# Optimization experiments

Measured on AMD Instinct MI355X. Metric: run time of the kernel, lower is better.

The kernel has to match this reference:

```python
import jax, jax.numpy as jnp
import numpy as np

STEPS = 3
TOP_N = 2
ROUTE_TEMP = 1.5


def setup_inputs() -> dict:
    key = jax.random.key(0)
    ks = jax.random.split(key, 7)
    B, H, W, C = 16, 112, 112, 128
    heads, dh = 2, 64
    hd = heads * dh  # 128
    K = 4
    s_in = 0.02  # keep activations well-scaled through 3 steps
    x = jax.random.normal(ks[0], (B, H, W, C), dtype=jnp.float32)
    Wk = jax.random.normal(ks[1], (C, hd), dtype=jnp.float32) * s_in
    Wv = jax.random.normal(ks[2], (C, hd), dtype=jnp.float32) * s_in
    q = jax.random.normal(ks[3], (heads, dh), dtype=jnp.float32) * 0.1
    Wmlp = jax.random.normal(ks[4], (hd, K), dtype=jnp.float32) * 0.1
    Wb = jax.random.normal(ks[5], (K, C, C), dtype=jnp.float32) * (1.0 / np.sqrt(C))
    alpha = jnp.zeros((), dtype=jnp.float32)  # attn_log_alpha
    return {"x": x, "Wk": Wk, "Wv": Wv, "q": q, "Wmlp": Wmlp, "Wb": Wb, "alpha": alpha}


def _router(x, Wk, Wv, q, Wmlp):
    # AttnPoolRouter: 1x1 conv K/V, single-query-per-head softmax attention pool.
    B, H, W, C = x.shape
    heads, dh = q.shape
    L = H * W
    k = jnp.einsum('bhwc,ce->bhwe', x, Wk).reshape(B, L, heads, dh)  # [B,L,h,d]
    v = jnp.einsum('bhwc,ce->bhwe', x, Wv).reshape(B, L, heads, dh)
    scores = jnp.einsum('hd,blhd->bhl', q, k) / jnp.sqrt(jnp.asarray(dh, x.dtype))
    attn = jax.nn.softmax(scores, axis=-1)                            # [B,h,L]
    pooled = jnp.einsum('bhl,blhd->bhd', attn, v).reshape(B, heads * dh)
    logits = pooled @ Wmlp                                            # [B,K]
    attn_map = attn.mean(axis=1).reshape(B, H, W, 1)                  # [B,H,W,1]
    return logits, attn_map


def reference(x, Wk, Wv, q, Wmlp, Wb, alpha):
    B, H, W, C = x.shape
    K = Wmlp.shape[1]
    scale = jnp.asarray(H * W, x.dtype)
    a = jax.nn.softplus(alpha)
    for _ in range(STEPS):
        logits, attn_map = _router(x, Wk, Wv, q, Wmlp)
        weights = jax.nn.softmax(logits / ROUTE_TEMP, axis=-1)        # [B,K]
        _, top_idx = jax.lax.top_k(weights, TOP_N)                    # [B,top_n]
        top_mask = jax.nn.one_hot(top_idx, K, dtype=weights.dtype).sum(axis=1)
        wm = weights * top_mask
        ws = wm / (wm.sum(axis=-1, keepdims=True) + 1e-9)
        # straight-through: forward = renormalized top-n, gradient flows to full softmax
        wst = ws + jax.lax.stop_gradient(weights - ws)                # [B,K]
        x_mod = x * (1.0 + attn_map * scale * a)                      # [B,H,W,C]
        # all K branch 1x1 convs, combined by straight-through weights
        x = jnp.einsum('bhwc,kcd,bk->bhwd', x_mod, Wb, wst)
    return x
```

## Files before the change

### kernel.cpp

```cpp
#include <hip/hip_runtime.h>
#include <hip/hip_bf16.h>
#include <cstdint>

#define NB 16
#define NC 128
#define NL 12544
#define NHD 128
#define NK 4
#define ROWS (NB*NL)
#define CH 128
#define PCH2 98

typedef unsigned short ushort_t;
typedef __attribute__((ext_vector_type(8))) short bf16x8;
typedef __attribute__((ext_vector_type(4))) float f32x4;

__device__ __forceinline__ float bf2f(unsigned int u){
  union { unsigned int i; float f; } v; v.i = u << 16; return v.f;
}
__device__ __forceinline__ ushort_t f2bf(float f){
  __hip_bfloat16 h = __float2bfloat16(f);
  return *reinterpret_cast<ushort_t*>(&h);
}

__global__ void k_prep(const float* __restrict__ Wk, const float* __restrict__ q,
                       const float* __restrict__ alpha, float* __restrict__ qk,
                       float* __restrict__ scale_a){
  int t = threadIdx.x;
  if (t < NC*2){
    int c = t >> 1, h = t & 1;
    float s = 0.f;
    for (int d = 0; d < 64; ++d) s += Wk[c*NHD + h*64 + d] * q[h*64 + d];
    qk[c*2 + h] = s * 0.125f;
  }
  if (t == 0){
    float a = alpha[0];
    float sp = (a > 20.f) ? a : log1pf(expf(a));
    *scale_a = (float)NL * sp;
  }
}

__global__ void __launch_bounds__(256,4) k_pass1(const float* __restrict__ x,
    const float* __restrict__ qk, float* __restrict__ sraw,
    float* __restrict__ pm, float* __restrict__ pS, float* __restrict__ pP){
  __shared__ __align__(16) ushort_t xs[CH*NC];
  __shared__ float shs0[CH], shs1[CH];
  __shared__ float red[8];
  __shared__ float pmerge[256];
  int wg = ((blockIdx.x & 7) * 196) + (blockIdx.x >> 3);
  int b = wg / PCH2, chunk = wg % PCH2;
  int l0 = chunk*CH;
  int t = threadIdx.x, lane = t & 63, wave = t >> 6;
  int hi = lane >> 4, n16 = lane & 15;

  {
    const float* src = x + ((size_t)b*NL + l0)*NC;
    #pragma unroll
    for (int i = 0; i < 16; ++i){
      int idx = i*1024 + t*4;
      int row = idx >> 7;
      float4 v = *(const float4*)(src + idx);
      unsigned p0 = (unsigned)f2bf(v.x) | ((unsigned)f2bf(v.y) << 16);
      unsigned p1 = (unsigned)f2bf(v.z) | ((unsigned)f2bf(v.w) << 16);
      *(uint2*)((char*)xs + ((idx*2) ^ ((row & 7) << 4))) = make_uint2(p0, p1);
    }
  }
  bf16x8 qfv[4];
  #pragma unroll
  for (int kk = 0; kk < 4; ++kk)
    #pragma unroll
    for (int j = 0; j < 8; ++j){
      int k = kk*32 + hi*8 + j;
      qfv[kk][j] = (n16 < 2) ? (short)f2bf(qk[k*2 + n16]) : (short)0;
    }
  __syncthreads();

  #pragma unroll
  for (int rt2 = 0; rt2 < 2; ++rt2){
    int rt = wave*2 + rt2;
    f32x4 acc = (f32x4){0.f,0.f,0.f,0.f};
    #pragma unroll
    for (int kk = 0; kk < 4; ++kk){
      int row = rt*16 + n16;
      int k = kk*32 + hi*8;
      bf16x8 a = *(const bf16x8*)((const char*)xs + ((row*256 + k*2) ^ ((row & 7) << 4)));
      acc = __builtin_amdgcn_mfma_f32_16x16x32_bf16(a, qfv[kk], acc, 0, 0, 0);
    }
    if (n16 < 2){
      float* dst = n16 ? shs1 : shs0;
      #pragma unroll
      for (int r = 0; r < 4; ++r) dst[rt*16 + hi*4 + r] = acc[r];
    }
  }
  __syncthreads();

  float s0 = -3.4e38f, s1 = -3.4e38f;
  if (t < 128){
    s0 = shs0[t]; s1 = shs1[t];
    sraw[((size_t)b*2+0)*NL + l0 + t] = s0;
    sraw[((size_t)b*2+1)*NL + l0 + t] = s1;
  }
  float m0 = s0, m1 = s1;
  #pragma unroll
  for (int mk = 32; mk; mk >>= 1){ m0 = fmaxf(m0, __shfl_xor(m0, mk)); m1 = fmaxf(m1, __shfl_xor(m1, mk)); }
  if (lane == 0 && wave < 2){ red[wave] = m0; red[2+wave] = m1; }
  __syncthreads();
  float M0 = fmaxf(red[0], red[1]), M1 = fmaxf(red[2], red[3]);
  float e0 = 0.f, e1 = 0.f;
  if (t < 128){ e0 = __expf(s0 - M0); e1 = __expf(s1 - M1); shs0[t] = e0; shs1[t] = e1; }
  float t0 = e0, t1 = e1;
  #pragma unroll
  for (int mk = 32; mk; mk >>= 1){ t0 += __shfl_xor(t0, mk); t1 += __shfl_xor(t1, mk); }
  if (lane == 0 && wave < 2){ red[4+wave] = t0; red[6+wave] = t1; }
  __syncthreads();
  if (t == 0){
    pm[(b*2+0)*PCH2 + chunk] = M0; pm[(b*2+1)*PCH2 + chunk] = M1;
    pS[(b*2+0)*PCH2 + chunk] = red[4]+red[5];
    pS[(b*2+1)*PCH2 + chunk] = red[6]+red[7];
  }

  int h = t >> 7, half = (t >> 6) & 1, cp = t & 63;
  const float* es = h ? shs1 : shs0;
  float a0 = 0.f, a1 = 0.f;
  #pragma unroll 4
  for (int i = 0; i < 64; ++i){
    int l = half*64 + i;
    float e = es[l];
    unsigned u = *(const unsigned*)((const char*)xs + ((l*256 + 4*cp) ^ ((l & 7) << 4)));
    a0 += e * bf2f(u & 0xffffu);
    a1 += e * bf2f(u >> 16);
  }
  __syncthreads();
  if (half){ pmerge[h*128 + cp*2] = a0; pmerge[h*128 + cp*2 + 1] = a1; }
  __syncthreads();
  if (!half){
    a0 += pmerge[h*128 + cp*2];
    a1 += pmerge[h*128 + cp*2 + 1];
    float2 w; w.x = a0; w.y = a1;
    *(float2*)&pP[(((size_t)b*PCH2 + chunk)*2 + h)*NC + 2*cp] = w;
  }
}

__global__ void k_combine(const float* __restrict__ pm, const float* __restrict__ pS,
    const float* __restrict__ pP, const float* __restrict__ Wv,
    const float* __restrict__ Wmlp, const float* __restrict__ Wb,
    ushort_t* __restrict__ WT, float* __restrict__ amS){
  int b = blockIdx.x, t = threadIdx.x, lane = t & 63, wave = t >> 6;
  __shared__ float w98[2][PCH2];
  __shared__ float pxs[2][NC];
  __shared__ float vpool[NHD];
  __shared__ float wts[NK];
  __shared__ float mSh[4];
  __shared__ float wcomb[NC*129];

  if (wave < 2){
    int h = wave;
    const float* pmh = pm + (b*2+h)*PCH2;
    const float* pSh = pS + (b*2+h)*PCH2;
    float m = -3.4e38f;
    for (int j = lane; j < PCH2; j += 64) m = fmaxf(m, pmh[j]);
    #pragma unroll
    for (int mk = 32; mk; mk >>= 1) m = fmaxf(m, __shfl_xor(m, mk));
    float S = 0.f;
    for (int j = lane; j < PCH2; j += 64) S += pSh[j] * __expf(pmh[j] - m);
    #pragma unroll
    for (int mk = 32; mk; mk >>= 1) S += __shfl_xor(S, mk);
    for (int j = lane; j < PCH2; j += 64) w98[h][j] = __expf(pmh[j] - m);
    if (lane == 0){
      float iS = 1.f/S;
      mSh[h] = m; mSh[2+h] = iS;
      amS[(b*2+h)*2 + 0] = m; amS[(b*2+h)*2 + 1] = iS;
    }
  }
  __syncthreads();
  {
    int h = t >> 7, c = t & 127;
    float s = 0.f;
    #pragma unroll 2
    for (int j = 0; j < PCH2; ++j) s += pP[(((size_t)b*PCH2 + j)*2 + h)*NC + c] * w98[h][j];
    pxs[h][c] = s * mSh[2+h];
  }
  __syncthreads();
  if (t < NHD){
    int h = t >> 6, d = t & 63;
    float s = 0.f;
    for (int c = 0; c < NC; ++c) s += pxs[h][c] * Wv[c*NHD + h*64 + d];
    vpool[t] = s;
  }
  __syncthreads();
  if (t < NK){
    float s = 0.f;
    for (int e = 0; e < NHD; ++e) s += vpool[e] * Wmlp[e*NK + t];
    wts[t] = s * (1.0f/1.5f);
  }
  __syncthreads();
  if (t == 0){
    float m = fmaxf(fmaxf(wts[0], wts[1]), fmaxf(wts[2], wts[3]));
    float e0 = __expf(wts[0]-m), e1 = __expf(wts[1]-m), e2 = __expf(wts[2]-m), e3 = __expf(wts[3]-m);
    float inv = 1.f/(e0+e1+e2+e3);
    wts[0] = e0*inv; wts[1] = e1*inv; wts[2] = e2*inv; wts[3] = e3*inv;
  }
  __syncthreads();
  float w0 = wts[0], w1 = wts[1], w2 = wts[2], w3 = wts[3];
  for (int idx = t; idx < NC*NC; idx += 256){
    int c = idx >> 7, d = idx & 127;
    const float* wb = Wb + (size_t)c*NC + d;
    wcomb[c*129 + d] = w0*wb[0] + w1*wb[NC*NC] + w2*wb[2*NC*NC] + w3*wb[3*NC*NC];
  }
  __syncthreads();
  for (int idx = t; idx < NC*NHD; idx += 256){
    int d = idx >> 7, c = idx & 127;
    WT[(size_t)b*NC*NHD + d*NC + c] = f2bf(wcomb[c*129 + d]);
  }
}

template<typename XIN, typename XOUT, bool STATS>
__global__ void __launch_bounds__(256,2) k_gemm(const XIN* __restrict__ xin,
    const ushort_t* __restrict__ WT, const float* __restrict__ qkg,
    float* __restrict__ sraw, const float* __restrict__ amS,
    const float* __restrict__ scale_a, XOUT* __restrict__ xout,
    float* __restrict__ pm, float* __restrict__ pS, float* __restrict__ pP){
  __shared__ __align__(16) ushort_t lA[CH*NC];
  __shared__ __align__(16) ushort_t lB[NC*NHD];
  __shared__ float sqk[256];
  __shared__ float shs0[CH], shs1[CH];
  __shared__ float red[8];
  __shared__ float pacc[4][2][NC];
  int wg = ((blockIdx.x & 7) * 196) + (blockIdx.x >> 3);
  int b = wg / PCH2, chunk = wg % PCH2;
  int l0 = chunk*CH;
  int t = threadIdx.x;
  float sa = scale_a[0]*0.5f;
  float am0 = amS[(b*2+0)*2+0], ai0 = amS[(b*2+0)*2+1];
  float am1 = amS[(b*2+1)*2+0], ai1 = amS[(b*2+1)*2+1];
  const float* s0p = sraw + ((size_t)b*2 + 0)*NL + l0;
  const float* s1p = sraw + ((size_t)b*2 + 1)*NL + l0;

  if (STATS){ sqk[t] = qkg[t]; }

  {
    const ushort_t* src = WT + (size_t)b*NC*NHD;
    #pragma unroll
    for (int i = 0; i < 8; ++i){
      int idx = i*2048 + t*8;
      int d = idx >> 7;
      uint4 v = *(const uint4*)(src + idx);
      *(uint4*)((char*)lB + ((idx*2) ^ ((d & 7) << 4))) = v;
    }
  }
  if constexpr (sizeof(XIN) == 4){
    const float* src = (const float*)xin + ((size_t)b*NL + l0)*NC;
    #pragma unroll
    for (int i = 0; i < 16; ++i){
      int idx = i*1024 + t*4;
      int row = idx >> 7;
      float4 v = *(const float4*)(src + idx);
      float mod = 1.f + sa*(__expf(s0p[row]-am0)*ai0 + __expf(s1p[row]-am1)*ai1);
      unsigned p0 = (unsigned)f2bf(v.x*mod) | ((unsigned)f2bf(v.y*mod) << 16);
      unsigned p1 = (unsigned)f2bf(v.z*mod) | ((unsigned)f2bf(v.w*mod) << 16);
      *(uint2*)((char*)lA + ((idx*2) ^ ((row & 7) << 4))) = make_uint2(p0, p1);
    }
  } else {
    const ushort_t* src = (const ushort_t*)xin + ((size_t)b*NL + l0)*NC;
    #pragma unroll
    for (int i = 0; i < 8; ++i){
      int idx = i*2048 + t*8;
      int row = idx >> 7;
      uint4 v = *(const uint4*)(src + idx);
      float mod = 1.f + sa*(__expf(s0p[row]-am0)*ai0 + __expf(s1p[row]-am1)*ai1);
      unsigned vv[4] = {v.x, v.y, v.z, v.w};
      unsigned r[4];
      #pragma unroll
      for (int j = 0; j < 4; ++j){
        float lo = bf2f(vv[j] & 0xffffu)*mod, hi2 = bf2f(vv[j] >> 16)*mod;
        r[j] = (unsigned)f2bf(lo) | ((unsigned)f2bf(hi2) << 16);
      }
      *(uint4*)((char*)lA + ((idx*2) ^ ((row & 7) << 4))) = make_uint4(r[0], r[1], r[2], r[3]);
    }
  }
  __syncthreads();

  int lane = t & 63, wave = t >> 6;
  int trow = lane & 15, kg = lane >> 4;
  int r0 = wave*32;
  f32x4 acc[2][8];
  #pragma unroll
  for (int m = 0; m < 2; ++m)
    #pragma unroll
    for (int n = 0; n < 8; ++n) acc[m][n] = (f32x4){0.f,0.f,0.f,0.f};

  #pragma unroll
  for (int kk = 0; kk < 4; ++kk){
    int k = kk*32 + kg*8;
    int ra0 = r0 + trow, ra1 = r0 + 16 + trow;
    bf16x8 a0 = *(const bf16x8*)((const char*)lA + ((ra0*256 + k*2) ^ ((ra0 & 7) << 4)));
    bf16x8 a1 = *(const bf16x8*)((const char*)lA + ((ra1*256 + k*2) ^ ((ra1 & 7) << 4)));
    #pragma unroll
    for (int nt = 0; nt < 8; ++nt){
      int col = nt*16 + trow;
      bf16x8 bf = *(const bf16x8*)((const char*)lB + ((col*256 + k*2) ^ ((col & 7) << 4)));
      acc[0][nt] = __builtin_amdgcn_mfma_f32_16x16x32_bf16(a0, bf, acc[0][nt], 0, 0, 0);
      acc[1][nt] = __builtin_amdgcn_mfma_f32_16x16x32_bf16(a1, bf, acc[1][nt], 0, 0, 0);
    }
  }

  size_t base = ((size_t)b*NL + l0)*NC;
  #pragma unroll
  for (int m = 0; m < 2; ++m)
    #pragma unroll
    for (int nt = 0; nt < 8; ++nt)
      #pragma unroll
      for (int r = 0; r < 4; ++r){
        int row = r0 + m*16 + kg*4 + r;
        int col = nt*16 + trow;
        float v = acc[m][nt][r];
        if constexpr (sizeof(XOUT) == 4) ((float*)xout)[base + (size_t)row*NC + col] = v;
        else                             ((ushort_t*)xout)[base + (size_t)row*NC + col] = f2bf(v);
      }

  if (STATS){
    float wq0[8], wq1[8];
    #pragma unroll
    for (int nt = 0; nt < 8; ++nt){
      wq0[nt] = sqk[(nt*16 + trow)*2 + 0];
      wq1[nt] = sqk[(nt*16 + trow)*2 + 1];
    }
    #pragma unroll
    for (int m = 0; m < 2; ++m)
      #pragma unroll
      for (int r = 0; r < 4; ++r){
        float p0 = 0.f, p1 = 0.f;
        #pragma unroll
        for (int nt = 0; nt < 8; ++nt){ float v = acc[m][nt][r]; p0 += v*wq0[nt]; p1 += v*wq1[nt]; }
        #pragma unroll
        for (int mk = 1; mk < 16; mk <<= 1){ p0 += __shfl_xor(p0, mk); p1 += __shfl_xor(p1, mk); }
        int idx = m*4 + r;
        if (trow == idx){
          int row = r0 + m*16 + kg*4 + r;
          shs0[row] = p0; shs1[row] = p1;
        }
      }
    __syncthreads();

    float s0 = -3.4e38f, s1 = -3.4e38f;
    if (t < 128){
      s0 = shs0[t]; s1 = shs1[t];
      sraw[((size_t)b*2+0)*NL + l0 + t] = s0;
      sraw[((size_t)b*2+1)*NL + l0 + t] = s1;
    }
    float m0 = s0, m1 = s1;
    #pragma unroll
    for (int mk = 32; mk; mk >>= 1){ m0 = fmaxf(m0, __shfl_xor(m0, mk)); m1 = fmaxf(m1, __shfl_xor(m1, mk)); }
    if (lane == 0 && wave < 2){ red[wave] = m0; red[2+wave] = m1; }
    __syncthreads();
    float M0 = fmaxf(red[0], red[1]), M1 = fmaxf(red[2], red[3]);
    float e0 = 0.f, e1 = 0.f;
    if (t < 128){ e0 = __expf(s0 - M0); e1 = __expf(s1 - M1); shs0[t] = e0; shs1[t] = e1; }
    float t0 = e0, t1 = e1;
    #pragma unroll
    for (int mk = 32; mk; mk >>= 1){ t0 += __shfl_xor(t0, mk); t1 += __shfl_xor(t1, mk); }
    if (lane == 0 && wave < 2){ red[4+wave] = t0; red[6+wave] = t1; }
    __syncthreads();
    if (t == 0){
      pm[(b*2+0)*PCH2 + chunk] = M0; pm[(b*2+1)*PCH2 + chunk] = M1;
      pS[(b*2+0)*PCH2 + chunk] = red[4]+red[5];
      pS[(b*2+1)*PCH2 + chunk] = red[6]+red[7];
    }

    float ea0[2][4], ea1[2][4];
    #pragma unroll
    for (int m = 0; m < 2; ++m)
      #pragma unroll
      for (int r = 0; r < 4; ++r){
        int row = r0 + m*16 + kg*4 + r;
        ea0[m][r] = shs0[row]; ea1[m][r] = shs1[row];
      }
    #pragma unroll
    for (int nt = 0; nt < 8; ++nt){
      float p0 = 0.f, p1 = 0.f;
      #pragma unroll
      for (int m = 0; m < 2; ++m)
        #pragma unroll
        for (int r = 0; r < 4; ++r){
          p0 += ea0[m][r]*acc[m][nt][r];
          p1 += ea1[m][r]*acc[m][nt][r];
        }
      p0 += __shfl_xor(p0, 16); p0 += __shfl_xor(p0, 32);
      p1 += __shfl_xor(p1, 16); p1 += __shfl_xor(p1, 32);
      int col = nt*16 + trow;
      if (kg == 0) pacc[wave][0][col] = p0;
      if (kg == 1) pacc[wave][1][col] = p1;
    }
    __syncthreads();
    {
      int h = t >> 7, c = t & 127;
      pP[(((size_t)b*PCH2 + chunk)*2 + h)*NC + c] =
        pacc[0][h][c] + pacc[1][h][c] + pacc[2][h][c] + pacc[3][h][c];
    }
  }
}

extern "C" void kernel_launch(void* const* d_in, const int* in_sizes, int n_in,
                              void* d_out, int out_size, void* d_ws, size_t ws_size,
                              hipStream_t stream){
  const float* x0   = (const float*)d_in[0];
  const float* Wk   = (const float*)d_in[1];
  const float* Wv   = (const float*)d_in[2];
  const float* q    = (const float*)d_in[3];
  const float* Wmlp = (const float*)d_in[4];
  const float* Wb   = (const float*)d_in[5];
  const float* alpha= (const float*)d_in[6];
  float* out = (float*)d_out;

  char* ws = (char*)d_ws;
  float* qk      = (float*)ws;
  float* scale_a = qk + 256;
  float* sraw    = qk + 320;
  float* pm      = sraw + (size_t)NB*2*NL;
  float* pS      = pm + NB*2*PCH2;
  float* pP      = pS + NB*2*PCH2;
  float* amS     = pP + (size_t)NB*PCH2*2*NC;
  ushort_t* WT   = (ushort_t*)(amS + NB*4);
  char* endfixed = (char*)(WT + (size_t)NB*NC*NHD);
  size_t xoff    = ((size_t)(endfixed - ws) + 255) & ~(size_t)255;
  ushort_t* xb   = (ushort_t*)(ws + xoff);
  bool big = ws_size >= xoff + (size_t)ROWS*NC*2;

  k_prep<<<1, 256, 0, stream>>>(Wk, q, alpha, qk, scale_a);

  k_pass1<<<NB*PCH2, 256, 0, stream>>>(x0, qk, sraw, pm, pS, pP);

  dim3 g(NB*PCH2);
  for (int step = 0; step < 3; ++step){
    k_combine<<<NB, 256, 0, stream>>>(pm, pS, pP, Wv, Wmlp, Wb, WT, amS);

    if (big){
      if (step == 0)
        k_gemm<float, ushort_t, true ><<<g, 256, 0, stream>>>(x0, WT, qk, sraw, amS, scale_a, xb, pm, pS, pP);
      else if (step == 1)
        k_gemm<ushort_t, ushort_t, true ><<<g, 256, 0, stream>>>(xb, WT, qk, sraw, amS, scale_a, xb, pm, pS, pP);
      else
        k_gemm<ushort_t, float, false><<<g, 256, 0, stream>>>(xb, WT, qk, sraw, amS, scale_a, out, pm, pS, pP);
    } else {
      if (step == 0)
        k_gemm<float, float, true ><<<g, 256, 0, stream>>>(x0, WT, qk, sraw, amS, scale_a, out, pm, pS, pP);
      else if (step == 1)
        k_gemm<float, float, true ><<<g, 256, 0, stream>>>(out, WT, qk, sraw, amS, scale_a, out, pm, pS, pP);
      else
        k_gemm<float, float, false><<<g, 256, 0, stream>>>(out, WT, qk, sraw, amS, scale_a, out, pm, pS, pP);
    }
  }
}
```

Before: 388.1 us.

## Fuse router combine into GEMM kernel with per-batch looping blocks

Removes the prep and combine kernels. Each GEMM block now recomputes its batch's attention-pool reduction, routing softmax and combined bf16 weight matrix in shared memory, then loops over its batch's spatial chunks. The attention modulation is applied as a per-row scale after the MFMA instead of while loading the input, and the partial stats are double-buffered between steps. This cuts kernel launches and the WT/amS round-trips, but every block redundantly reads Wb and the partial sums, and each block works through several chunks with no overlap between them.

New measurement: 400.4 us. +3.2%, slower.

```diff
diff --git a/kernel.cpp b/kernel.cpp
--- a/kernel.cpp
+++ b/kernel.cpp
@@ -15,40 +15,24 @@
 typedef __attribute__((ext_vector_type(8))) short bf16x8;
 typedef __attribute__((ext_vector_type(4))) float f32x4;
 
-__device__ __forceinline__ float bf2f(unsigned int u){
-  union { unsigned int i; float f; } v; v.i = u << 16; return v.f;
+__device__ __forceinline__ float bf2f(unsigned u){
+  union { unsigned i; float f; } v; v.i = u << 16; return v.f;
 }
 __device__ __forceinline__ ushort_t f2bf(float f){
-  __hip_bfloat16 h = __float2bfloat16(f);
-  return *reinterpret_cast<ushort_t*>(&h);
+  unsigned u = __float_as_uint(f);
+  return (ushort_t)((u + 0x7FFFu + ((u >> 16) & 1u)) >> 16);
 }
 
-__global__ void k_prep(const float* __restrict__ Wk, const float* __restrict__ q,
-                       const float* __restrict__ alpha, float* __restrict__ qk,
-                       float* __restrict__ scale_a){
-  int t = threadIdx.x;
-  if (t < NC*2){
-    int c = t >> 1, h = t & 1;
-    float s = 0.f;
-    for (int d = 0; d < 64; ++d) s += Wk[c*NHD + h*64 + d] * q[h*64 + d];
-    qk[c*2 + h] = s * 0.125f;
-  }
-  if (t == 0){
-    float a = alpha[0];
-    float sp = (a > 20.f) ? a : log1pf(expf(a));
-    *scale_a = (float)NL * sp;
-  }
-}
-
 __global__ void __launch_bounds__(256,4) k_pass1(const float* __restrict__ x,
-    const float* __restrict__ qk, float* __restrict__ sraw,
-    float* __restrict__ pm, float* __restrict__ pS, float* __restrict__ pP){
+    const float* __restrict__ Wk, const float* __restrict__ q,
+    float* __restrict__ sraw, float* __restrict__ pm, float* __restrict__ pS,
+    float* __restrict__ pP){
   __shared__ __align__(16) ushort_t xs[CH*NC];
+  __shared__ float sqk[NC*2];
   __shared__ float shs0[CH], shs1[CH];
   __shared__ float red[8];
   __shared__ float pmerge[256];
-  int wg = ((blockIdx.x & 7) * 196) + (blockIdx.x >> 3);
-  int b = wg / PCH2, chunk = wg % PCH2;
+  int b = blockIdx.x / PCH2, chunk = blockIdx.x % PCH2;
   int l0 = chunk*CH;
   int t = threadIdx.x, lane = t & 63, wave = t >> 6;
   int hi = lane >> 4, n16 = lane & 15;
@@ -65,15 +49,23 @@
       *(uint2*)((char*)xs + ((idx*2) ^ ((row & 7) << 4))) = make_uint2(p0, p1);
     }
   }
+  {
+    int c = t >> 1, h = t & 1;
+    float s = 0.f;
+    #pragma unroll 8
+    for (int d = 0; d < 64; ++d) s += Wk[c*NHD + h*64 + d] * q[h*64 + d];
+    sqk[c*2 + h] = s * 0.125f;
+  }
+  __syncthreads();
+
   bf16x8 qfv[4];
   #pragma unroll
   for (int kk = 0; kk < 4; ++kk)
     #pragma unroll
     for (int j = 0; j < 8; ++j){
       int k = kk*32 + hi*8 + j;
-      qfv[kk][j] = (n16 < 2) ? (short)f2bf(qk[k*2 + n16]) : (short)0;
-    }
-  __syncthreads();
+      qfv[kk][j] = (n16 < 2) ? (short)f2bf(sqk[k*2 + n16]) : (short)0;
+    }
 
   #pragma unroll
   for (int rt2 = 0; rt2 < 2; ++rt2){
@@ -141,22 +133,45 @@
   }
 }
 
-__global__ void k_combine(const float* __restrict__ pm, const float* __restrict__ pS,
-    const float* __restrict__ pP, const float* __restrict__ Wv,
+template<typename XIN, typename XOUT, bool STATS>
+__global__ void __launch_bounds__(256,2) k_gemm(const XIN* __restrict__ xin,
+    const float* __restrict__ Wk, const float* __restrict__ q,
+    const float* __restrict__ alpha, const float* __restrict__ Wv,
     const float* __restrict__ Wmlp, const float* __restrict__ Wb,
-    ushort_t* __restrict__ WT, float* __restrict__ amS){
-  int b = blockIdx.x, t = threadIdx.x, lane = t & 63, wave = t >> 6;
+    float* __restrict__ sraw,
+    const float* __restrict__ pmR, const float* __restrict__ pSR, const float* __restrict__ pPR,
+    float* __restrict__ pmW, float* __restrict__ pSW, float* __restrict__ pPW,
+    XOUT* __restrict__ xout){
+  __shared__ __align__(16) ushort_t lA[CH*NC];
+  __shared__ __align__(16) ushort_t lB[NC*NHD];
+  __shared__ float sqk[NC*2];
   __shared__ float w98[2][PCH2];
   __shared__ float pxs[2][NC];
   __shared__ float vpool[NHD];
   __shared__ float wts[NK];
   __shared__ float mSh[4];
-  __shared__ float wcomb[NC*129];
-
+  __shared__ float shmod[CH];
+  __shared__ float shs0[CH], shs1[CH];
+  __shared__ float red[8];
+  __shared__ float pacc[4][2][NC];
+  int b = blockIdx.x >> 5, part = blockIdx.x & 31;
+  int t = threadIdx.x, lane = t & 63, wave = t >> 6;
+
+  float av = alpha[0];
+  float sp = (av > 20.f) ? av : log1pf(__expf(av));
+  float sa = (float)NL * sp * 0.5f;
+
+  if (STATS){
+    int c = t >> 1, h = t & 1;
+    float s = 0.f;
+    #pragma unroll 8
+    for (int d = 0; d < 64; ++d) s += Wk[c*NHD + h*64 + d] * q[h*64 + d];
+    sqk[c*2 + h] = s * 0.125f;
+  }
   if (wave < 2){
     int h = wave;
-    const float* pmh = pm + (b*2+h)*PCH2;
-    const float* pSh = pS + (b*2+h)*PCH2;
+    const float* pmh = pmR + (b*2+h)*PCH2;
+    const float* pSh = pSR + (b*2+h)*PCH2;
     float m = -3.4e38f;
     for (int j = lane; j < PCH2; j += 64) m = fmaxf(m, pmh[j]);
     #pragma unroll
@@ -166,18 +181,14 @@
     #pragma unroll
     for (int mk = 32; mk; mk >>= 1) S += __shfl_xor(S, mk);
     for (int j = lane; j < PCH2; j += 64) w98[h][j] = __expf(pmh[j] - m);
-    if (lane == 0){
-      float iS = 1.f/S;
-      mSh[h] = m; mSh[2+h] = iS;
-      amS[(b*2+h)*2 + 0] = m; amS[(b*2+h)*2 + 1] = iS;
-    }
+    if (lane == 0){ mSh[h] = m; mSh[2+h] = 1.f/S; }
   }
   __syncthreads();
   {
     int h = t >> 7, c = t & 127;
     float s = 0.f;
     #pragma unroll 2
-    for (int j = 0; j < PCH2; ++j) s += pP[(((size_t)b*PCH2 + j)*2 + h)*NC + c] * w98[h][j];
+    for (int j = 0; j < PCH2; ++j) s += pPR[(((size_t)b*PCH2 + j)*2 + h)*NC + c] * w98[h][j];
     pxs[h][c] = s * mSh[2+h];
   }
   __syncthreads();
@@ -188,214 +199,181 @@
     vpool[t] = s;
   }
   __syncthreads();
-  if (t < NK){
-    float s = 0.f;
-    for (int e = 0; e < NHD; ++e) s += vpool[e] * Wmlp[e*NK + t];
-    wts[t] = s * (1.0f/1.5f);
-  }
-  __syncthreads();
-  if (t == 0){
-    float m = fmaxf(fmaxf(wts[0], wts[1]), fmaxf(wts[2], wts[3]));
-    float e0 = __expf(wts[0]-m), e1 = __expf(wts[1]-m), e2 = __expf(wts[2]-m), e3 = __expf(wts[3]-m);
-    float inv = 1.f/(e0+e1+e2+e3);
-    wts[0] = e0*inv; wts[1] = e1*inv; wts[2] = e2*inv; wts[3] = e3*inv;
-  }
-  __syncthreads();
-  float w0 = wts[0], w1 = wts[1], w2 = wts[2], w3 = wts[3];
-  for (int idx = t; idx < NC*NC; idx += 256){
-    int c = idx >> 7, d = idx & 127;
-    const float* wb = Wb + (size_t)c*NC + d;
-    wcomb[c*129 + d] = w0*wb[0] + w1*wb[NC*NC] + w2*wb[2*NC*NC] + w3*wb[3*NC*NC];
-  }
-  __syncthreads();
-  for (int idx = t; idx < NC*NHD; idx += 256){
-    int d = idx >> 7, c = idx & 127;
-    WT[(size_t)b*NC*NHD + d*NC + c] = f2bf(wcomb[c*129 + d]);
-  }
-}
-
-template<typename XIN, typename XOUT, bool STATS>
-__global__ void __launch_bounds__(256,2) k_gemm(const XIN* __restrict__ xin,
-    const ushort_t* __restrict__ WT, const float* __restrict__ qkg,
-    float* __restrict__ sraw, const float* __restrict__ amS,
-    const float* __restrict__ scale_a, XOUT* __restrict__ xout,
-    float* __restrict__ pm, float* __restrict__ pS, float* __restrict__ pP){
-  __shared__ __align__(16) ushort_t lA[CH*NC];
-  __shared__ __align__(16) ushort_t lB[NC*NHD];
-  __shared__ float sqk[256];
-  __shared__ float shs0[CH], shs1[CH];
-  __shared__ float red[8];
-  __shared__ float pacc[4][2][NC];
-  int wg = ((blockIdx.x & 7) * 196) + (blockIdx.x >> 3);
-  int b = wg / PCH2, chunk = wg % PCH2;
-  int l0 = chunk*CH;
-  int t = threadIdx.x;
-  float sa = scale_a[0]*0.5f;
-  float am0 = amS[(b*2+0)*2+0], ai0 = amS[(b*2+0)*2+1];
-  float am1 = amS[(b*2+1)*2+0], ai1 = amS[(b*2+1)*2+1];
-  const float* s0p = sraw + ((size_t)b*2 + 0)*NL + l0;
-  const float* s1p = sraw + ((size_t)b*2 + 1)*NL + l0;
-
-  if (STATS){ sqk[t] = qkg[t]; }
-
+  if (t < 64){
+    float lg = 0.f;
+    if (lane < 4){
+      for (int e = 0; e < NHD; ++e) lg += vpool[e] * Wmlp[e*NK + lane];
+      lg *= (1.0f/1.5f);
+    }
+    float m01 = fmaxf(lg, __shfl_xor(lg, 1));
+    float mall = fmaxf(m01, __shfl_xor(m01, 2));
+    float e = __expf(lg - mall);
+    float s01 = e + __shfl_xor(e, 1);
+    float sall = s01 + __shfl_xor(s01, 2);
+    if (lane < 4) wts[lane] = e / sall;
+  }
+  __syncthreads();
   {
-    const ushort_t* src = WT + (size_t)b*NC*NHD;
-    #pragma unroll
-    for (int i = 0; i < 8; ++i){
-      int idx = i*2048 + t*8;
-      int d = idx >> 7;
-      uint4 v = *(const uint4*)(src + idx);
-      *(uint4*)((char*)lB + ((idx*2) ^ ((d & 7) << 4))) = v;
-    }
-  }
-  if constexpr (sizeof(XIN) == 4){
-    const float* src = (const float*)xin + ((size_t)b*NL + l0)*NC;
-    #pragma unroll
-    for (int i = 0; i < 16; ++i){
-      int idx = i*1024 + t*4;
-      int row = idx >> 7;
-      float4 v = *(const float4*)(src + idx);
-      float mod = 1.f + sa*(__expf(s0p[row]-am0)*ai0 + __expf(s1p[row]-am1)*ai1);
-      unsigned p0 = (unsigned)f2bf(v.x*mod) | ((unsigned)f2bf(v.y*mod) << 16);
-      unsigned p1 = (unsigned)f2bf(v.z*mod) | ((unsigned)f2bf(v.w*mod) << 16);
-      *(uint2*)((char*)lA + ((idx*2) ^ ((row & 7) << 4))) = make_uint2(p0, p1);
-    }
-  } else {
-    const ushort_t* src = (const ushort_t*)xin + ((size_t)b*NL + l0)*NC;
-    #pragma unroll
-    for (int i = 0; i < 8; ++i){
-      int idx = i*2048 + t*8;
-      int row = idx >> 7;
-      uint4 v = *(const uint4*)(src + idx);
-      float mod = 1.f + sa*(__expf(s0p[row]-am0)*ai0 + __expf(s1p[row]-am1)*ai1);
-      unsigned vv[4] = {v.x, v.y, v.z, v.w};
-      unsigned r[4];
-      #pragma unroll
-      for (int j = 0; j < 4; ++j){
-        float lo = bf2f(vv[j] & 0xffffu)*mod, hi2 = bf2f(vv[j] >> 16)*mod;
-        r[j] = (unsigned)f2bf(lo) | ((unsigned)f2bf(hi2) << 16);
-      }
-      *(uint4*)((char*)lA + ((idx*2) ^ ((row & 7) << 4))) = make_uint4(r[0], r[1], r[2], r[3]);
-    }
-  }
-  __syncthreads();
-
-  int lane = t & 63, wave = t >> 6;
-  int trow = lane & 15, kg = lane >> 4;
-  int r0 = wave*32;
-  f32x4 acc[2][8];
-  #pragma unroll
-  for (int m = 0; m < 2; ++m)
-    #pragma unroll
-    for (int n = 0; n < 8; ++n) acc[m][n] = (f32x4){0.f,0.f,0.f,0.f};
-
-  #pragma unroll
-  for (int kk = 0; kk < 4; ++kk){
-    int k = kk*32 + kg*8;
-    int ra0 = r0 + trow, ra1 = r0 + 16 + trow;
-    bf16x8 a0 = *(const bf16x8*)((const char*)lA + ((ra0*256 + k*2) ^ ((ra0 & 7) << 4)));
-    bf16x8 a1 = *(const bf16x8*)((const char*)lA + ((ra1*256 + k*2) ^ ((ra1 & 7) << 4)));
-    #pragma unroll
-    for (int nt = 0; nt < 8; ++nt){
-      int col = nt*16 + trow;
-      bf16x8 bf = *(const bf16x8*)((const char*)lB + ((col*256 + k*2) ^ ((col & 7) << 4)));
-      acc[0][nt] = __builtin_amdgcn_mfma_f32_16x16x32_bf16(a0, bf, acc[0][nt], 0, 0, 0);
-      acc[1][nt] = __builtin_amdgcn_mfma_f32_16x16x32_bf16(a1, bf, acc[1][nt], 0, 0, 0);
-    }
-  }
-
-  size_t base = ((size_t)b*NL + l0)*NC;
-  #pragma unroll
-  for (int m = 0; m < 2; ++m)
-    #pragma unroll
-    for (int nt = 0; nt < 8; ++nt)
-      #pragma unroll
-      for (int r = 0; r < 4; ++r){
-        int row = r0 + m*16 + kg*4 + r;
+    float w0 = wts[0], w1 = wts[1], w2 = wts[2], w3 = wts[3];
+    for (int idx = t; idx < NC*NC; idx += 256){
+      int c = idx >> 7, d = idx & 127;
+      const float* wb = Wb + (size_t)c*NC + d;
+      float v = w0*wb[0] + w1*wb[NC*NC] + w2*wb[2*NC*NC] + w3*wb[3*NC*NC];
+      *(ushort_t*)((char*)lB + ((d*256 + c*2) ^ ((d & 7) << 4))) = f2bf(v);
+    }
+  }
+
+  int trow = lane & 15, kg = lane >> 4, r0 = wave*32;
+  for (int ci = part; ci < PCH2; ci += 32){
+    int l0 = ci*CH;
+    const float* s0p = sraw + ((size_t)b*2 + 0)*NL + l0;
+    const float* s1p = sraw + ((size_t)b*2 + 1)*NL + l0;
+    __syncthreads();
+
+    if constexpr (sizeof(XIN) == 4){
+      const float* src = (const float*)xin + ((size_t)b*NL + l0)*NC;
+      #pragma unroll
+      for (int i = 0; i < 16; ++i){
+        int idx = i*1024 + t*4;
+        int row = idx >> 7;
+        float4 v = *(const float4*)(src + idx);
+        unsigned p0 = (unsigned)f2bf(v.x) | ((unsigned)f2bf(v.y) << 16);
+        unsigned p1 = (unsigned)f2bf(v.z) | ((unsigned)f2bf(v.w) << 16);
+        *(uint2*)((char*)lA + ((idx*2) ^ ((row & 7) << 4))) = make_uint2(p0, p1);
+      }
+    } else {
+      const ushort_t* src = (const ushort_t*)xin + ((size_t)b*NL + l0)*NC;
+      #pragma unroll
+      for (int i = 0; i < 8; ++i){
+        int idx = i*2048 + t*8;
+        int row = idx >> 7;
+        uint4 v = *(const uint4*)(src + idx);
+        *(uint4*)((char*)lA + ((idx*2) ^ ((row & 7) << 4))) = v;
+      }
+    }
+    if (t < CH)
+      shmod[t] = 1.f + sa*(__expf(s0p[t]-mSh[0])*mSh[2] + __expf(s1p[t]-mSh[1])*mSh[3]);
+    __syncthreads();
+
+    f32x4 acc[2][8];
+    #pragma unroll
+    for (int m = 0; m < 2; ++m)
+      #pragma unroll
+      for (int n = 0; n < 8; ++n) acc[m][n] = (f32x4){0.f,0.f,0.f,0.f};
+    #pragma unroll
+    for (int kk = 0; kk < 4; ++kk){
+      int k = kk*32 + kg*8;
+      int ra0 = r0 + trow, ra1 = r0 + 16 + trow;
+      bf16x8 a0 = *(const bf16x8*)((const char*)lA + ((ra0*256 + k*2) ^ ((ra0 & 7) << 4)));
+      bf16x8 a1 = *(const bf16x8*)((const char*)lA + ((ra1*256 + k*2) ^ ((ra1 & 7) << 4)));
+      #pragma unroll
+      for (int nt = 0; nt < 8; ++nt){
         int col = nt*16 + trow;
-        float v = acc[m][nt][r];
-        if constexpr (sizeof(XOUT) == 4) ((float*)xout)[base + (size_t)row*NC + col] = v;
-        else                             ((ushort_t*)xout)[base + (size_t)row*NC + col] = f2bf(v);
-      }
-
-  if (STATS){
-    float wq0[8], wq1[8];
-    #pragma unroll
-    for (int nt = 0; nt < 8; ++nt){
-      wq0[nt] = sqk[(nt*16 + trow)*2 + 0];
-      wq1[nt] = sqk[(nt*16 + trow)*2 + 1];
-    }
+        bf16x8 bf = *(const bf16x8*)((const char*)lB + ((col*256 + k*2) ^ ((col & 7) << 4)));
+        acc[0][nt] = __builtin_amdgcn_mfma_f32_16x16x32_bf16(a0, bf, acc[0][nt], 0, 0, 0);
+        acc[1][nt] = __builtin_amdgcn_mfma_f32_16x16x32_bf16(a1, bf, acc[1][nt], 0, 0, 0);
+      }
+    }
+
+    float md[2][4];
     #pragma unroll
     for (int m = 0; m < 2; ++m)
       #pragma unroll
-      for (int r = 0; r < 4; ++r){
-        float p0 = 0.f, p1 = 0.f;
+      for (int r = 0; r < 4; ++r) md[m][r] = shmod[r0 + m*16 + kg*4 + r];
+
+    size_t base = ((size_t)b*NL + l0)*NC;
+    #pragma unroll
+    for (int m = 0; m < 2; ++m)
+      #pragma unroll
+      for (int nt = 0; nt < 8; ++nt)
         #pragma unroll
-        for (int nt = 0; nt < 8; ++nt){ float v = acc[m][nt][r]; p0 += v*wq0[nt]; p1 += v*wq1[nt]; }
-        #pragma unroll
-        for (int mk = 1; mk < 16; mk <<= 1){ p0 += __shfl_xor(p0, mk); p1 += __shfl_xor(p1, mk); }
-        int idx = m*4 + r;
-        if (trow == idx){
+        for (int r = 0; r < 4; ++r){
           int row = r0 + m*16 + kg*4 + r;
-          shs0[row] = p0; shs1[row] = p1;
+          int col = nt*16 + trow;
+          float v = acc[m][nt][r] * md[m][r];
+          if constexpr (sizeof(XOUT) == 4) ((float*)xout)[base + (size_t)row*NC + col] = v;
+          else                             ((ushort_t*)xout)[base + (size_t)row*NC + col] = f2bf(v);
         }
-      }
-    __syncthreads();
-
-    float s0 = -3.4e38f, s1 = -3.4e38f;
-    if (t < 128){
-      s0 = shs0[t]; s1 = shs1[t];
-      sraw[((size_t)b*2+0)*NL + l0 + t] = s0;
-      sraw[((size_t)b*2+1)*NL + l0 + t] = s1;
-    }
-    float m0 = s0, m1 = s1;
-    #pragma unroll
-    for (int mk = 32; mk; mk >>= 1){ m0 = fmaxf(m0, __shfl_xor(m0, mk)); m1 = fmaxf(m1, __shfl_xor(m1, mk)); }
-    if (lane == 0 && wave < 2){ red[wave] = m0; red[2+wave] = m1; }
-    __syncthreads();
-    float M0 = fmaxf(red[0], red[1]), M1 = fmaxf(red[2], red[3]);
-    float e0 = 0.f, e1 = 0.f;
-    if (t < 128){ e0 = __expf(s0 - M0); e1 = __expf(s1 - M1); shs0[t] = e0; shs1[t] = e1; }
-    float t0 = e0, t1 = e1;
-    #pragma unroll
-    for (int mk = 32; mk; mk >>= 1){ t0 += __shfl_xor(t0, mk); t1 += __shfl_xor(t1, mk); }
-    if (lane == 0 && wave < 2){ red[4+wave] = t0; red[6+wave] = t1; }
-    __syncthreads();
-    if (t == 0){
-      pm[(b*2+0)*PCH2 + chunk] = M0; pm[(b*2+1)*PCH2 + chunk] = M1;
-      pS[(b*2+0)*PCH2 + chunk] = red[4]+red[5];
-      pS[(b*2+1)*PCH2 + chunk] = red[6]+red[7];
-    }
-
-    float ea0[2][4], ea1[2][4];
-    #pragma unroll
-    for (int m = 0; m < 2; ++m)
-      #pragma unroll
-      for (int r = 0; r < 4; ++r){
-        int row = r0 + m*16 + kg*4 + r;
-        ea0[m][r] = shs0[row]; ea1[m][r] = shs1[row];
-      }
-    #pragma unroll
-    for (int nt = 0; nt < 8; ++nt){
-      float p0 = 0.f, p1 = 0.f;
+
+    if (STATS){
+      float wq0[8], wq1[8];
+      #pragma unroll
+      for (int nt = 0; nt < 8; ++nt){
+        wq0[nt] = sqk[(nt*16 + trow)*2 + 0];
+        wq1[nt] = sqk[(nt*16 + trow)*2 + 1];
+      }
       #pragma unroll
       for (int m = 0; m < 2; ++m)
         #pragma unroll
         for (int r = 0; r < 4; ++r){
-          p0 += ea0[m][r]*acc[m][nt][r];
-          p1 += ea1[m][r]*acc[m][nt][r];
+          float p0 = 0.f, p1 = 0.f;
+          #pragma unroll
+          for (int nt = 0; nt < 8; ++nt){ float v = acc[m][nt][r]; p0 += v*wq0[nt]; p1 += v*wq1[nt]; }
+          #pragma unroll
+          for (int mk = 1; mk < 16; mk <<= 1){ p0 += __shfl_xor(p0, mk); p1 += __shfl_xor(p1, mk); }
+          int idx = m*4 + r;
+          if (trow == idx){
+            int row = r0 + m*16 + kg*4 + r;
+            shs0[row] = p0 * md[m][r]; shs1[row] = p1 * md[m][r];
+          }
         }
-      p0 += __shfl_xor(p0, 16); p0 += __shfl_xor(p0, 32);
-      p1 += __shfl_xor(p1, 16); p1 += __shfl_xor(p1, 32);
-      int col = nt*16 + trow;
-      if (kg == 0) pacc[wave][0][col] = p0;
-      if (kg == 1) pacc[wave][1][col] = p1;
-    }
-    __syncthreads();
-    {
-      int h = t >> 7, c = t & 127;
-      pP[(((size_t)b*PCH2 + chunk)*2 + h)*NC + c] =
-        pacc[0][h][c] + pacc[1][h][c] + pacc[2][h][c] + pacc[3][h][c];
+      __syncthreads();
+
+      float s0 = -3.4e38f, s1 = -3.4e38f;
+      if (t < 128){
+        s0 = shs0[t]; s1 = shs1[t];
+        sraw[((size_t)b*2+0)*NL + l0 + t] = s0;
+        sraw[((size_t)b*2+1)*NL + l0 + t] = s1;
+      }
+      float m0 = s0, m1 = s1;
+      #pragma unroll
+      for (int mk = 32; mk; mk >>= 1){ m0 = fmaxf(m0, __shfl_xor(m0, mk)); m1 = fmaxf(m1, __shfl_xor(m1, mk)); }
+      if (lane == 0 && wave < 2){ red[wave] = m0; red[2+wave] = m1; }
+      __syncthreads();
+      float M0 = fmaxf(red[0], red[1]), M1 = fmaxf(red[2], red[3]);
+      float e0 = 0.f, e1 = 0.f;
+      if (t < 128){ e0 = __expf(s0 - M0); e1 = __expf(s1 - M1); shs0[t] = e0; shs1[t] = e1; }
+      float t0 = e0, t1 = e1;
+      #pragma unroll
+      for (int mk = 32; mk; mk >>= 1){ t0 += __shfl_xor(t0, mk); t1 += __shfl_xor(t1, mk); }
+      if (lane == 0 && wave < 2){ red[4+wave] = t0; red[6+wave] = t1; }
+      __syncthreads();
+      if (t == 0){
+        pmW[(b*2+0)*PCH2 + ci] = M0; pmW[(b*2+1)*PCH2 + ci] = M1;
+        pSW[(b*2+0)*PCH2 + ci] = red[4]+red[5];
+        pSW[(b*2+1)*PCH2 + ci] = red[6]+red[7];
+      }
+
+      float ea0[2][4], ea1[2][4];
+      #pragma unroll
+      for (int m = 0; m < 2; ++m)
+        #pragma unroll
+        for (int r = 0; r < 4; ++r){
+          int row = r0 + m*16 + kg*4 + r;
+          ea0[m][r] = shs0[row] * md[m][r]; ea1[m][r] = shs1[row] * md[m][r];
+        }
+      #pragma unroll
+      for (int nt = 0; nt < 8; ++nt){
+        float p0 = 0.f, p1 = 0.f;
+        #pragma unroll
+        for (int m = 0; m < 2; ++m)
+          #pragma unroll
+          for (int r = 0; r < 4; ++r){
+            p0 += ea0[m][r]*acc[m][nt][r];
+            p1 += ea1[m][r]*acc[m][nt][r];
+          }
+        p0 += __shfl_xor(p0, 16); p0 += __shfl_xor(p0, 32);
+        p1 += __shfl_xor(p1, 16); p1 += __shfl_xor(p1, 32);
+        int col = nt*16 + trow;
+        if (kg == 0) pacc[wave][0][col] = p0;
+        if (kg == 1) pacc[wave][1][col] = p1;
+      }
+      __syncthreads();
+      {
+        int h = t >> 7, c = t & 127;
+        pPW[(((size_t)b*PCH2 + ci)*2 + h)*NC + c] =
+          pacc[0][h][c] + pacc[1][h][c] + pacc[2][h][c] + pacc[3][h][c];
+      }
     }
   }
 }
@@ -413,41 +391,34 @@
   float* out = (float*)d_out;
 
   char* ws = (char*)d_ws;
-  float* qk      = (float*)ws;
-  float* scale_a = qk + 256;
-  float* sraw    = qk + 320;
-  float* pm      = sraw + (size_t)NB*2*NL;
-  float* pS      = pm + NB*2*PCH2;
-  float* pP      = pS + NB*2*PCH2;
-  float* amS     = pP + (size_t)NB*PCH2*2*NC;
-  ushort_t* WT   = (ushort_t*)(amS + NB*4);
-  char* endfixed = (char*)(WT + (size_t)NB*NC*NHD);
-  size_t xoff    = ((size_t)(endfixed - ws) + 255) & ~(size_t)255;
-  ushort_t* xb   = (ushort_t*)(ws + xoff);
+  float* sraw = (float*)ws;
+  float* pmA  = sraw + (size_t)NB*2*NL;
+  float* pSA  = pmA + NB*2*PCH2;
+  float* pmB  = pSA + NB*2*PCH2;
+  float* pSB  = pmB + NB*2*PCH2;
+  float* pPA  = pSB + NB*2*PCH2;
+  float* pPB  = pPA + (size_t)NB*PCH2*2*NC;
+  char* endf  = (char*)(pPB + (size_t)NB*PCH2*2*NC);
+  size_t xoff = ((size_t)(endf - ws) + 255) & ~(size_t)255;
+  ushort_t* xb = (ushort_t*)(ws + xoff);
   bool big = ws_size >= xoff + (size_t)ROWS*NC*2;
 
-  k_prep<<<1, 256, 0, stream>>>(Wk, q, alpha, qk, scale_a);
-
-  k_pass1<<<NB*PCH2, 256, 0, stream>>>(x0, qk, sraw, pm, pS, pP);
-
-  dim3 g(NB*PCH2);
-  for (int step = 0; step < 3; ++step){
-    k_combine<<<NB, 256, 0, stream>>>(pm, pS, pP, Wv, Wmlp, Wb, WT, amS);
-
-    if (big){
-      if (step == 0)
-        k_gemm<float, ushort_t, true ><<<g, 256, 0, stream>>>(x0, WT, qk, sraw, amS, scale_a, xb, pm, pS, pP);
-      else if (step == 1)
-        k_gemm<ushort_t, ushort_t, true ><<<g, 256, 0, stream>>>(xb, WT, qk, sraw, amS, scale_a, xb, pm, pS, pP);
-      else
-        k_gemm<ushort_t, float, false><<<g, 256, 0, stream>>>(xb, WT, qk, sraw, amS, scale_a, out, pm, pS, pP);
-    } else {
-      if (step == 0)
-        k_gemm<float, float, true ><<<g, 256, 0, stream>>>(x0, WT, qk, sraw, amS, scale_a, out, pm, pS, pP);
-      else if (step == 1)
-        k_gemm<float, float, true ><<<g, 256, 0, stream>>>(out, WT, qk, sraw, amS, scale_a, out, pm, pS, pP);
-      else
-        k_gemm<float, float, false><<<g, 256, 0, stream>>>(out, WT, qk, sraw, amS, scale_a, out, pm, pS, pP);
-    }
+  k_pass1<<<NB*PCH2, 256, 0, stream>>>(x0, Wk, q, sraw, pmA, pSA, pPA);
+
+  dim3 g(NB*32);
+  if (big){
+    k_gemm<float,    ushort_t, true ><<<g, 256, 0, stream>>>(x0, Wk, q, alpha, Wv, Wmlp, Wb,
+        sraw, pmA, pSA, pPA, pmB, pSB, pPB, xb);
+    k_gemm<ushort_t, ushort_t, true ><<<g, 256, 0, stream>>>(xb, Wk, q, alpha, Wv, Wmlp, Wb,
+        sraw, pmB, pSB, pPB, pmA, pSA, pPA, xb);
+    k_gemm<ushort_t, float,    false><<<g, 256, 0, stream>>>(xb, Wk, q, alpha, Wv, Wmlp, Wb,
+        sraw, pmA, pSA, pPA, pmB, pSB, pPB, out);
+  } else {
+    k_gemm<float, float, true ><<<g, 256, 0, stream>>>(x0, Wk, q, alpha, Wv, Wmlp, Wb,
+        sraw, pmA, pSA, pPA, pmB, pSB, pPB, out);
+    k_gemm<float, float, true ><<<g, 256, 0, stream>>>(out, Wk, q, alpha, Wv, Wmlp, Wb,
+        sraw, pmB, pSB, pPB, pmA, pSA, pPA, out);
+    k_gemm<float, float, false><<<g, 256, 0, stream>>>(out, Wk, q, alpha, Wv, Wmlp, Wb,
+        sraw, pmA, pSA, pPA, pmB, pSB, pPB, out);
   }
 }
```
